# Optimization experiments

Measured on AMD Instinct MI355X. Metric: run time of the kernel, lower is better.

## Reference

```python
import jax, jax.numpy as jnp
import numpy as np

IN_F = 8192
OUT_F = 8192
TOKENS = 4096
QP = 127.0   # 2**(8-1) - 1
QN = -128.0  # -2**(8-1)


def setup_inputs() -> dict:
    key = jax.random.key(0)
    k1, k2 = jax.random.split(key)
    x = jax.random.normal(k1, (TOKENS, IN_F), dtype=jnp.float32)
    # torch.randint(0, 2, ...) -> values in {0, 1}
    weight = jax.random.randint(k2, (OUT_F, IN_F), 0, 2, dtype=jnp.int32)
    weight_scale = jnp.ones((1,), dtype=jnp.float32)
    bias = jnp.zeros((OUT_F,), dtype=jnp.float32)
    return {"x": x, "weight": weight, "weight_scale": weight_scale, "bias": bias}


def reference(x, weight, weight_scale, bias):
    # activation_quant: per-row symmetric int8 quantization
    s = QP / jnp.clip(jnp.max(jnp.abs(x), axis=-1, keepdims=True), 1e-5)  # [T,1]
    x_q = jnp.clip(jnp.round(x * s), QN, QP)  # int8 values held in f32 (exact)
    y = jnp.einsum('tk,nk->tn', x_q, weight.astype(x.dtype))  # [T, OUT_F]
    # post_quant_process: dequantize by activation scale then weight scale
    out = y / s / weight_scale
    return out + bias[None, :]
```

## Files before the change

kernel.cpp:

```cpp
#include <hip/hip_runtime.h>

#define TOKENS 4096
#define IN_F   8192
#define OUT_F  8192

typedef int v4i __attribute__((ext_vector_type(4)));

__device__ __forceinline__ void gload_lds16(const void* g, void* l) {
    __builtin_amdgcn_global_load_lds(
        (const __attribute__((address_space(1))) void*)g,
        (__attribute__((address_space(3))) void*)l, 16, 0, 0);
}

__global__ __launch_bounds__(256) void quant_kernel(const float* __restrict__ x,
                                                    signed char* __restrict__ xq,
                                                    float* __restrict__ recip_s) {
    const int row = blockIdx.x;
    const int t   = threadIdx.x;
    const float4* xr = (const float4*)(x + (size_t)row * IN_F);
    float4 v[8];
    float m = 0.f;
#pragma unroll
    for (int i = 0; i < 8; ++i) {
        v[i] = xr[t + 256 * i];
        m = fmaxf(m, fmaxf(fmaxf(fabsf(v[i].x), fabsf(v[i].y)),
                           fmaxf(fabsf(v[i].z), fabsf(v[i].w))));
    }
#pragma unroll
    for (int off = 32; off > 0; off >>= 1)
        m = fmaxf(m, __shfl_xor(m, off));
    __shared__ float wmax[4];
    if ((t & 63) == 0) wmax[t >> 6] = m;
    __syncthreads();
    m = fmaxf(fmaxf(wmax[0], wmax[1]), fmaxf(wmax[2], wmax[3]));
    m = fmaxf(m, 1e-5f);
    const float s = 127.0f / m;
    if (t == 0) recip_s[row] = m / 127.0f;
    unsigned int* out = (unsigned int*)(xq + (size_t)row * IN_F);
#pragma unroll
    for (int i = 0; i < 8; ++i) {
        int a = (int)fminf(fmaxf(rintf(v[i].x * s), -128.f), 127.f);
        int b = (int)fminf(fmaxf(rintf(v[i].y * s), -128.f), 127.f);
        int c = (int)fminf(fmaxf(rintf(v[i].z * s), -128.f), 127.f);
        int d = (int)fminf(fmaxf(rintf(v[i].w * s), -128.f), 127.f);
        out[t + 256 * i] = (a & 255) | ((b & 255) << 8) | ((c & 255) << 16) | ((d & 255) << 24);
    }
}

__global__ __launch_bounds__(256) void pack_w(const int* __restrict__ w,
                                              unsigned int* __restrict__ w8) {
    const size_t idx = (size_t)blockIdx.x * 256 + threadIdx.x;
    int4 a = ((const int4*)w)[idx];
    w8[idx] = (a.x & 255) | ((a.y & 255) << 8) | ((a.z & 255) << 16) | ((a.w & 255) << 24);
}

__global__ __launch_bounds__(256, 2) void gemm_kernel(const signed char* __restrict__ A,
                                                      const signed char* __restrict__ B,
                                                      const float* __restrict__ recip_s,
                                                      const float* __restrict__ wscale,
                                                      const float* __restrict__ bias,
                                                      float* __restrict__ out) {
    __shared__ signed char As[2 * 128 * 64];
    __shared__ signed char Bs[2 * 256 * 64];
    const int t    = threadIdx.x;
    const int wave = t >> 6;
    const int lane = t & 63;
    const int m0 = blockIdx.y * 128;
    const int n0 = blockIdx.x * 256;
    const int wm = (wave >> 1) * 64;
    const int wn = (wave & 1) * 128;

    v4i acc[4][8] = {};

    const int rowS = t >> 2;
    const int colS = ((t & 3) ^ ((t >> 3) & 3)) * 16;
    const signed char* gA = A + (size_t)(m0 + rowS) * IN_F + colS;
    const signed char* gB = B + (size_t)(n0 + rowS) * IN_F + colS;
    signed char* lA = As + t * 16;
    signed char* lB = Bs + t * 16;

    const int r16 = lane & 15;
    const int q   = lane >> 4;
    const int cOff = ((q ^ ((r16 >> 1) & 3)) * 16);

    gload_lds16(gA, lA);
    gload_lds16(gA + (size_t)64 * IN_F, lA + 4096);
    gload_lds16(gB, lB);
    gload_lds16(gB + (size_t)64 * IN_F, lB + 4096);
    gload_lds16(gB + (size_t)128 * IN_F, lB + 8192);
    gload_lds16(gB + (size_t)192 * IN_F, lB + 12288);

    int buf = 0;
    for (int k0 = 0; k0 < IN_F; k0 += 64) {
        const int kn = k0 + 64;
        if (kn < IN_F) {
            signed char* nA = lA + (buf ^ 1) * 8192;
            signed char* nB = lB + (buf ^ 1) * 16384;
            gload_lds16(gA + kn, nA);
            gload_lds16(gA + (size_t)64 * IN_F + kn, nA + 4096);
            gload_lds16(gB + kn, nB);
            gload_lds16(gB + (size_t)64 * IN_F + kn, nB + 4096);
            gload_lds16(gB + (size_t)128 * IN_F + kn, nB + 8192);
            gload_lds16(gB + (size_t)192 * IN_F + kn, nB + 12288);
            asm volatile("s_waitcnt vmcnt(6) lgkmcnt(0)" ::: "memory");
        } else {
            asm volatile("s_waitcnt vmcnt(0) lgkmcnt(0)" ::: "memory");
        }
        asm volatile("s_barrier" ::: "memory");

        const signed char* pA = As + buf * 8192;
        const signed char* pB = Bs + buf * 16384;
        v4i a[4], b[8];
#pragma unroll
        for (int i = 0; i < 4; ++i)
            a[i] = *(const v4i*)(pA + (wm + i * 16 + r16) * 64 + cOff);
#pragma unroll
        for (int j = 0; j < 8; ++j)
            b[j] = *(const v4i*)(pB + (wn + j * 16 + r16) * 64 + cOff);
#pragma unroll
        for (int i = 0; i < 4; ++i)
#pragma unroll
            for (int j = 0; j < 8; ++j)
                acc[i][j] = __builtin_amdgcn_mfma_i32_16x16x64_i8(a[i], b[j], acc[i][j], 0, 0, 0);

        asm volatile("s_waitcnt lgkmcnt(0)" ::: "memory");
        asm volatile("s_barrier" ::: "memory");
        buf ^= 1;
    }

    const float rws = 1.0f / wscale[0];
#pragma unroll
    for (int i = 0; i < 4; ++i) {
#pragma unroll
        for (int r = 0; r < 4; ++r) {
            const int row = m0 + wm + i * 16 + q * 4 + r;
            const float rs = recip_s[row] * rws;
#pragma unroll
            for (int j = 0; j < 8; ++j) {
                const int col = n0 + wn + j * 16 + r16;
                out[(size_t)row * OUT_F + col] = (float)acc[i][j][r] * rs + bias[col];
            }
        }
    }
}

extern "C" void kernel_launch(void* const* d_in, const int* in_sizes, int n_in,
                              void* d_out, int out_size, void* d_ws, size_t ws_size,
                              hipStream_t stream) {
    const float* x      = (const float*)d_in[0];
    const int*   w      = (const int*)d_in[1];
    const float* wscale = (const float*)d_in[2];
    const float* bias   = (const float*)d_in[3];
    float* out = (float*)d_out;

    signed char* xq = (signed char*)d_ws;
    signed char* w8 = xq + (size_t)TOKENS * IN_F;
    float* recip_s  = (float*)(w8 + (size_t)OUT_F * IN_F);

    quant_kernel<<<TOKENS, 256, 0, stream>>>(x, xq, recip_s);
    pack_w<<<(int)(((size_t)OUT_F * IN_F) / 4 / 256), 256, 0, stream>>>(w, (unsigned int*)w8);
    dim3 grid(OUT_F / 256, TOKENS / 128);
    gemm_kernel<<<grid, 256, 0, stream>>>(xq, w8, recip_s, wscale, bias, out);
}
```

Measured before the change: 740.4 us.

## Enlarge GEMM tile to 256x256 and switch to 32x32x32 int8 MFMA

The block tile grows from 128x256 to 256x256, so each wave computes a 128x128 sub-tile using 32x32x32 i8 MFMA instructions with 16-wide accumulators instead of 16x16x64. This raises arithmetic intensity per LDS byte loaded and cuts the LDS fragment reads per MFMA. In exchange, occupancy drops to one block per CU because of the larger LDS footprint and register usage, and the grid halves in the M dimension, which risks poorer latency hiding and load balance.

```diff
diff --git a/kernel.cpp b/kernel.cpp
--- a/kernel.cpp
+++ b/kernel.cpp
@@ -4,7 +4,8 @@
 #define IN_F   8192
 #define OUT_F  8192
 
-typedef int v4i __attribute__((ext_vector_type(4)));
+typedef int v4i  __attribute__((ext_vector_type(4)));
+typedef int v16i __attribute__((ext_vector_type(16)));
 
 __device__ __forceinline__ void gload_lds16(const void* g, void* l) {
     __builtin_amdgcn_global_load_lds(
@@ -54,23 +55,23 @@
     w8[idx] = (a.x & 255) | ((a.y & 255) << 8) | ((a.z & 255) << 16) | ((a.w & 255) << 24);
 }
 
-__global__ __launch_bounds__(256, 2) void gemm_kernel(const signed char* __restrict__ A,
+__global__ __launch_bounds__(256, 1) void gemm_kernel(const signed char* __restrict__ A,
                                                       const signed char* __restrict__ B,
                                                       const float* __restrict__ recip_s,
                                                       const float* __restrict__ wscale,
                                                       const float* __restrict__ bias,
                                                       float* __restrict__ out) {
-    __shared__ signed char As[2 * 128 * 64];
+    __shared__ signed char As[2 * 256 * 64];
     __shared__ signed char Bs[2 * 256 * 64];
     const int t    = threadIdx.x;
     const int wave = t >> 6;
     const int lane = t & 63;
-    const int m0 = blockIdx.y * 128;
+    const int m0 = blockIdx.y * 256;
     const int n0 = blockIdx.x * 256;
-    const int wm = (wave >> 1) * 64;
+    const int wm = (wave >> 1) * 128;
     const int wn = (wave & 1) * 128;
 
-    v4i acc[4][8] = {};
+    v16i acc[4][4] = {};
 
     const int rowS = t >> 2;
     const int colS = ((t & 3) ^ ((t >> 3) & 3)) * 16;
@@ -79,49 +80,53 @@
     signed char* lA = As + t * 16;
     signed char* lB = Bs + t * 16;
 
-    const int r16 = lane & 15;
-    const int q   = lane >> 4;
-    const int cOff = ((q ^ ((r16 >> 1) & 3)) * 16);
+    const int rl = lane & 31;
+    const int q  = lane >> 5;
+    const int sw = (rl >> 1) & 3;
+    const int c0 = ((0 + 2 * 0 + q) ^ sw) * 16;
+    const int c1 = ((2 + q) ^ sw) * 16;
 
-    gload_lds16(gA, lA);
-    gload_lds16(gA + (size_t)64 * IN_F, lA + 4096);
-    gload_lds16(gB, lB);
-    gload_lds16(gB + (size_t)64 * IN_F, lB + 4096);
-    gload_lds16(gB + (size_t)128 * IN_F, lB + 8192);
-    gload_lds16(gB + (size_t)192 * IN_F, lB + 12288);
+#pragma unroll
+    for (int c = 0; c < 4; ++c) {
+        gload_lds16(gA + (size_t)(c * 64) * IN_F, lA + c * 4096);
+        gload_lds16(gB + (size_t)(c * 64) * IN_F, lB + c * 4096);
+    }
 
     int buf = 0;
     for (int k0 = 0; k0 < IN_F; k0 += 64) {
         const int kn = k0 + 64;
         if (kn < IN_F) {
-            signed char* nA = lA + (buf ^ 1) * 8192;
+            signed char* nA = lA + (buf ^ 1) * 16384;
             signed char* nB = lB + (buf ^ 1) * 16384;
-            gload_lds16(gA + kn, nA);
-            gload_lds16(gA + (size_t)64 * IN_F + kn, nA + 4096);
-            gload_lds16(gB + kn, nB);
-            gload_lds16(gB + (size_t)64 * IN_F + kn, nB + 4096);
-            gload_lds16(gB + (size_t)128 * IN_F + kn, nB + 8192);
-            gload_lds16(gB + (size_t)192 * IN_F + kn, nB + 12288);
-            asm volatile("s_waitcnt vmcnt(6) lgkmcnt(0)" ::: "memory");
+#pragma unroll
+            for (int c = 0; c < 4; ++c) {
+                gload_lds16(gA + (size_t)(c * 64) * IN_F + kn, nA + c * 4096);
+                gload_lds16(gB + (size_t)(c * 64) * IN_F + kn, nB + c * 4096);
+            }
+            asm volatile("s_waitcnt vmcnt(8) lgkmcnt(0)" ::: "memory");
         } else {
             asm volatile("s_waitcnt vmcnt(0) lgkmcnt(0)" ::: "memory");
         }
         asm volatile("s_barrier" ::: "memory");
 
-        const signed char* pA = As + buf * 8192;
-        const signed char* pB = Bs + buf * 16384;
-        v4i a[4], b[8];
+        const signed char* pA = As + buf * 16384 + (wm + rl) * 64;
+        const signed char* pB = Bs + buf * 16384 + (wn + rl) * 64;
 #pragma unroll
-        for (int i = 0; i < 4; ++i)
-            a[i] = *(const v4i*)(pA + (wm + i * 16 + r16) * 64 + cOff);
+        for (int ks = 0; ks < 2; ++ks) {
+            const int cb = ks ? c1 : c0;
+            v4i a[4], b[4];
 #pragma unroll
-        for (int j = 0; j < 8; ++j)
-            b[j] = *(const v4i*)(pB + (wn + j * 16 + r16) * 64 + cOff);
+            for (int i = 0; i < 4; ++i)
+                a[i] = *(const v4i*)(pA + i * 32 * 64 + cb);
 #pragma unroll
-        for (int i = 0; i < 4; ++i)
+            for (int j = 0; j < 4; ++j)
+                b[j] = *(const v4i*)(pB + j * 32 * 64 + cb);
 #pragma unroll
-            for (int j = 0; j < 8; ++j)
-                acc[i][j] = __builtin_amdgcn_mfma_i32_16x16x64_i8(a[i], b[j], acc[i][j], 0, 0, 0);
+            for (int i = 0; i < 4; ++i)
+#pragma unroll
+                for (int j = 0; j < 4; ++j)
+                    acc[i][j] = __builtin_amdgcn_mfma_i32_32x32x32_i8(a[i], b[j], acc[i][j], 0, 0, 0);
+        }
 
         asm volatile("s_waitcnt lgkmcnt(0)" ::: "memory");
         asm volatile("s_barrier" ::: "memory");
@@ -129,16 +134,17 @@
     }
 
     const float rws = 1.0f / wscale[0];
+    const int colBase = n0 + wn + rl;
 #pragma unroll
     for (int i = 0; i < 4; ++i) {
 #pragma unroll
-        for (int r = 0; r < 4; ++r) {
-            const int row = m0 + wm + i * 16 + q * 4 + r;
+        for (int reg = 0; reg < 16; ++reg) {
+            const int row = m0 + wm + i * 32 + (reg & 3) + 8 * (reg >> 2) + 4 * q;
             const float rs = recip_s[row] * rws;
 #pragma unroll
-            for (int j = 0; j < 8; ++j) {
-                const int col = n0 + wn + j * 16 + r16;
-                out[(size_t)row * OUT_F + col] = (float)acc[i][j][r] * rs + bias[col];
+            for (int j = 0; j < 4; ++j) {
+                const int col = colBase + j * 32;
+                out[(size_t)row * OUT_F + col] = (float)acc[i][j][reg] * rs + bias[col];
             }
         }
     }
@@ -159,6 +165,6 @@
 
     quant_kernel<<<TOKENS, 256, 0, stream>>>(x, xq, recip_s);
     pack_w<<<(int)(((size_t)OUT_F * IN_F) / 4 / 256), 256, 0, stream>>>(w, (unsigned int*)w8);
-    dim3 grid(OUT_F / 256, TOKENS / 128);
+    dim3 grid(OUT_F / 256, TOKENS / 256);
     gemm_kernel<<<grid, 256, 0, stream>>>(xq, w8, recip_s, wscale, bias, out);
 }
```

After: 908.5 us. +22.7%, slower.
